# Kernel tuning notes

Hardware: AMD Instinct MI355X
Metric: run time of the kernel (lower is better)

The kernel has to match this reference:

```python
import jax, jax.numpy as jnp
import numpy as np
from jax import lax

EPS_CSA = 1e-5
EPS_BN = 1e-5


def _csa(x, w, pm_pos, ps_pos, pm_neg, ps_neg, label):
    # x: [B,C,H,W]; w: [B,K]; proto tables: [K,C]; label: [B] in {0,1}
    mean = jnp.mean(x, axis=(2, 3), keepdims=True)
    var = jnp.var(x, axis=(2, 3), ddof=1, keepdims=True)  # torch.var is unbiased
    mean = lax.stop_gradient(mean)
    var = lax.stop_gradient(var)
    x_norm = (x - mean) / jnp.sqrt(var + EPS_CSA)
    sel = (label == 0)[:, None]                       # [B,1]
    new_mean = jnp.where(sel, w @ pm_pos, w @ pm_neg)  # [B,C]
    new_std = jnp.where(sel, w @ ps_pos, w @ ps_neg)   # [B,C]
    return x_norm * new_std[:, :, None, None] + new_mean[:, :, None, None]


def _conv_bn(x, conv_w, gamma, beta):
    y = lax.conv_general_dilated(x, conv_w, (1, 1), 'SAME',
                                 dimension_numbers=('NCHW', 'OIHW', 'NCHW'))
    mu = jnp.mean(y, axis=(0, 2, 3), keepdims=True)
    var = jnp.var(y, axis=(0, 2, 3), keepdims=True)  # biased var, as BN training
    yn = (y - mu) / jnp.sqrt(var + EPS_BN)
    return yn * gamma[None, :, None, None] + beta[None, :, None, None]


def setup_inputs() -> dict:
    key = jax.random.key(0)
    ks = jax.random.split(key, 10)
    B, C, H, W, K, L = 32, 384, 32, 32, 64, 2
    conc = jnp.full((K,), 0.0156, dtype=jnp.float32)
    cw = jax.random.dirichlet(ks[5], conc, shape=(L, B)).astype(jnp.float32)
    return {
        'x': jax.random.normal(ks[0], (B, C, H, W), jnp.float32),
        'proto_mean_pos': jax.random.normal(ks[1], (L, K, C), jnp.float32),
        'proto_std_pos': jax.random.uniform(ks[2], (L, K, C), jnp.float32),
        'proto_mean_neg': jax.random.normal(ks[3], (L, K, C), jnp.float32),
        'proto_std_neg': jax.random.uniform(ks[4], (L, K, C), jnp.float32),
        'combine_weights': cw,
        'conv_w': jax.random.normal(ks[6], (C, C, 3, 3), jnp.float32) * (1.0 / np.sqrt(C * 9)),
        'bn_gamma': jnp.ones((C,), jnp.float32),
        'bn_beta': jnp.zeros((C,), jnp.float32),
        'label': jax.random.randint(ks[7], (B,), 0, 2, jnp.int32),
    }


def reference(x, proto_mean_pos, proto_std_pos, proto_mean_neg, proto_std_neg,
              combine_weights, conv_w, bn_gamma, bn_beta, label):
    fea = x
    for l in range(2):  # two CSABlocks: x + CSA(x, label)
        fea = fea + _csa(fea, combine_weights[l],
                         proto_mean_pos[l], proto_std_pos[l],
                         proto_mean_neg[l], proto_std_neg[l], label)
    out_feat = _conv_bn(fea, conv_w, bn_gamma, bn_beta)
    return out_feat
```

## Files before the change

kernel.cpp:

```cpp
#include <hip/hip_runtime.h>
#include <stdint.h>

using f32x4  = __attribute__((ext_vector_type(4))) float;
using short8 = __attribute__((ext_vector_type(8))) short;

#define DEVI static __device__ __forceinline__

DEVI unsigned short f2bf(float f) {
  unsigned u = __float_as_uint(f);
  u += 0x7FFFu + ((u >> 16) & 1u);
  return (unsigned short)(u >> 16);
}

DEVI void gld16(const void* g, void* l) {
  __builtin_amdgcn_global_load_lds(
      reinterpret_cast<const __attribute__((address_space(1))) unsigned int*>(
          reinterpret_cast<uintptr_t>(g)),
      reinterpret_cast<__attribute__((address_space(3))) unsigned int*>(
          reinterpret_cast<uintptr_t>(l)),
      16, 0, 0);
}

__global__ void k_zero(float* __restrict__ bn, float* __restrict__ zp) {
  const int t = threadIdx.x;
  for (int i = t; i < 768; i += 256) bn[i] = 0.0f;
  for (int i = t; i < 1024; i += 256) zp[i] = 0.0f;
}

__global__ __launch_bounds__(256) void k_stats(const float* __restrict__ x,
                                               float* __restrict__ sums,
                                               float* __restrict__ sumsq) {
  const int bc = blockIdx.x;
  const float4 v =
      reinterpret_cast<const float4*>(x + (size_t)bc * 1024)[threadIdx.x];
  float s = v.x + v.y + v.z + v.w;
  float q = v.x * v.x + v.y * v.y + v.z * v.z + v.w * v.w;
#pragma unroll
  for (int off = 1; off < 64; off <<= 1) {
    s += __shfl_xor(s, off, 64);
    q += __shfl_xor(q, off, 64);
  }
  __shared__ float ls[4], lq[4];
  const int wv = threadIdx.x >> 6;
  if ((threadIdx.x & 63) == 0) { ls[wv] = s; lq[wv] = q; }
  __syncthreads();
  if (threadIdx.x == 0) {
    sums[bc]  = ls[0] + ls[1] + ls[2] + ls[3];
    sumsq[bc] = lq[0] + lq[1] + lq[2] + lq[3];
  }
}

__global__ __launch_bounds__(384) void k_coef(
    const float* __restrict__ pmp, const float* __restrict__ psp,
    const float* __restrict__ pmn, const float* __restrict__ psn,
    const float* __restrict__ cw, const int* __restrict__ label,
    const float* __restrict__ sums, const float* __restrict__ sumsq,
    float* __restrict__ Ac, float* __restrict__ Bc) {
  const int b = blockIdx.x;
  const int c = threadIdx.x;
  __shared__ float w0[64], w1[64];
  if (threadIdx.x < 64) w0[threadIdx.x] = cw[b * 64 + threadIdx.x];
  else if (threadIdx.x < 128) w1[threadIdx.x - 64] = cw[2048 + b * 64 + (threadIdx.x - 64)];
  __syncthreads();
  const bool sel = (label[b] == 0);
  const float* m1t = (sel ? pmp : pmn);
  const float* s1t = (sel ? psp : psn);
  const float* m2t = m1t + 64 * 384;
  const float* s2t = s1t + 64 * 384;
  float m1 = 0.f, s1 = 0.f, m2 = 0.f, s2 = 0.f;
  for (int k = 0; k < 64; ++k) {
    const float a0 = w0[k], a1 = w1[k];
    m1 += a0 * m1t[k * 384 + c];
    s1 += a0 * s1t[k * 384 + c];
    m2 += a1 * m2t[k * 384 + c];
    s2 += a1 * s2t[k * 384 + c];
  }
  const int bc = b * 384 + c;
  const float sum = sums[bc], sq = sumsq[bc];
  const float mean = sum * (1.0f / 1024.0f);
  float var = (sq - sum * mean) * (1.0f / 1023.0f);
  var = fmaxf(var, 0.0f);
  const float sd1 = sqrtf(var + 1e-5f);
  const float a1c = 1.0f + s1 / sd1;
  const float b1c = m1 - mean * (s1 / sd1);
  const float mean1 = a1c * mean + b1c;
  const float var1  = a1c * a1c * var;
  const float sd2 = sqrtf(var1 + 1e-5f);
  const float t2 = 1.0f + s2 / sd2;
  Ac[bc] = a1c * t2;
  Bc[bc] = b1c * t2 + m2 - mean1 * (s2 / sd2);
}

__global__ __launch_bounds__(256) void k_fea(const float* __restrict__ x,
                                             const float* __restrict__ Ac,
                                             const float* __restrict__ Bc,
                                             unsigned short* __restrict__ fea) {
  __shared__ unsigned short tb[256][68];
  const int t = threadIdx.x;
  const int g0 = blockIdx.x << 8;
  const int b = g0 >> 10;
  const int c0 = blockIdx.y * 64;
  const float* xb = x + (((size_t)b * 384) << 10) + (g0 & 1023) + t;
  const float* Ab = Ac + b * 384 + c0;
  const float* Bb = Bc + b * 384 + c0;
#pragma unroll 1
  for (int u8 = 0; u8 < 64; u8 += 8) {
    union { unsigned short us[8]; uint4 v; } pk;
#pragma unroll
    for (int u = 0; u < 8; ++u) {
      const int c = u8 + u;
      pk.us[u] = f2bf(Ab[c] * xb[(size_t)(c0 + c) << 10] + Bb[c]);
    }
    *reinterpret_cast<uint4*>(&tb[t][u8]) = pk.v;
  }
  __syncthreads();
  const int j = t & 7;
#pragma unroll
  for (int rep = 0; rep < 8; ++rep) {
    const int p = rep * 32 + (t >> 3);
    const uint4 v = *reinterpret_cast<const uint4*>(&tb[p][j * 8]);
    *reinterpret_cast<uint4*>(fea + (size_t)(g0 + p) * 384 + c0 + j * 8) = v;
  }
}

__global__ __launch_bounds__(256) void k_wcvt(const float* __restrict__ w,
                                              unsigned short* __restrict__ wb2) {
  const int g = blockIdx.x * 256 + threadIdx.x;
  const int ct = g / 41472;
  const int r1 = g - ct * 41472;
  const int step = r1 / 1152;
  const int r2 = r1 - step * 1152;
  const int slab = r2 >> 6;
  const int lane = r2 & 63;
  const int cc = step / 3, dy = step - cc * 3;
  const int r = slab * 16 + (lane >> 2);
  const int dxl = r / 96, co_l = r - dxl * 96;
  const int dd = (lane & 3) ^ ((co_l >> 1) & 3);
  const int tap = dy * 3 + dxl;
  const int co = ct * 96 + co_l;
  const int cib = cc * 32 + dd * 8;
  union { unsigned short us[8]; uint4 v4; } pk;
#pragma unroll
  for (int u = 0; u < 8; ++u)
    pk.us[u] = f2bf(w[(size_t)(co * 384 + cib + u) * 9 + tap]);
  *reinterpret_cast<uint4*>(wb2 + (size_t)g * 8) = pk.v4;
}

__global__ __launch_bounds__(256, 1) void k_conv(
    const unsigned short* __restrict__ fea, const unsigned short* __restrict__ wb2,
    const unsigned short* __restrict__ zpg, float* __restrict__ out,
    float* __restrict__ bn_sum, float* __restrict__ bn_sq) {
  __shared__ __align__(16) unsigned char lds[129024];
  const int tid = threadIdx.x;
  const int lane = tid & 63, wv = tid >> 6;
  const int pt = blockIdx.x;
  const int ct = blockIdx.y;
  const int b = pt >> 1, h0 = (pt & 1) * 16;
  const int co0 = ct * 96;
  const int wn = wv;

  const int l15 = lane & 15, d = lane >> 4;
  const int aoff = l15 * 64 + ((d ^ ((l15 >> 1) & 3)) << 4);
  int baddr[8][3];
  bool ok0[8], ok2[8];
#pragma unroll
  for (int n = 0; n < 8; ++n) {
    const int p_out = wn * 128 + n * 16 + l15;
    const int r_out = p_out >> 5, c_out = p_out & 31;
    ok0[n] = (c_out >= 1);
    ok2[n] = (c_out <= 30);
#pragma unroll
    for (int dx = 0; dx < 3; ++dx) {
      const int c = c_out + dx - 1;
      const int cs = ((unsigned)c < 32u) ? c : c_out;
      const int row = r_out * 32 + cs;
      baddr[n][dx] = row * 64 + ((d ^ ((row >> 1) & 3)) << 4);
    }
  }

  const unsigned short* wp = wb2 + (size_t)ct * 331776 + lane * 8;
#define WSTAGE(wo)                                                  \
  do {                                                              \
    gld16(wp + wv * 512,          lds + (wo) + wv * 1024);          \
    gld16(wp + wv * 512 + 2048,   lds + (wo) + wv * 1024 + 4096);   \
    gld16(wp + wv * 512 + 4096,   lds + (wo) + wv * 1024 + 8192);   \
    gld16(wp + wv * 512 + 6144,   lds + (wo) + wv * 1024 + 12288);  \
    if (wv < 2)                                                     \
      gld16(wp + wv * 512 + 8192, lds + (wo) + wv * 1024 + 16384);  \
    wp += 9216;                                                     \
  } while (0)

  const unsigned short* ip[9];
  int istep[9];
#pragma unroll
  for (int dy2 = 0; dy2 < 3; ++dy2) {
#pragma unroll
    for (int k = 0; k < 3; ++k) {
      const int j = dy2 * 3 + k;
      const int s = dy2 * 12 + wv + 4 * k;
      const int pix = s * 16 + (lane >> 2);
      const int prow = pix >> 5, pcol = pix & 31;
      const int h = h0 - 1 + prow;
      const int dd = (lane & 3) ^ ((pix >> 1) & 3);
      if (h >= 0 && h < 32) {
        ip[j] = fea + ((size_t)((b * 32 + h) * 32 + pcol) * 384 + dd * 8);
        istep[j] = 32;
      } else {
        ip[j] = zpg + lane * 8;
        istep[j] = 0;
      }
    }
  }

  f32x4 acc[6][8] = {};
  const short8 z8 = {0, 0, 0, 0, 0, 0, 0, 0};
  short8 pf_af[6], pf_bf[8];

  WSTAGE(0);
  WSTAGE(18432);
#pragma unroll
  for (int j = 0; j < 9; ++j) {
    const int dy2 = j / 3, k = j - dy2 * 3;
    const int s = dy2 * 12 + wv + 4 * k;
    gld16(ip[j], lds + 55296 + s * 1024);
    ip[j] += istep[j];
  }
  __syncthreads();
#pragma unroll
  for (int m = 0; m < 6; ++m)
    pf_af[m] = *reinterpret_cast<const short8*>(lds + m * 1024 + aoff);

  for (int cc = 0; cc < 12; ++cc) {
#pragma unroll
    for (int dy = 0; dy < 3; ++dy) {
      const int st = cc * 3 + dy;
      const unsigned char* wbase = lds + dy * 18432;
      const unsigned char* wnext = lds + ((dy + 1) % 3) * 18432;
      const unsigned char* ibase = lds + 55296 + (cc & 1) * 36864;
      if (cc < 11 || dy == 0) WSTAGE(((dy + 2) % 3) * 18432);
      if (cc < 11) {
        const int io = 55296 + ((cc + 1) & 1) * 36864;
        const int s0 = dy * 12 + wv;
#pragma unroll
        for (int k = 0; k < 3; ++k) {
          const int j = dy * 3 + k;
          gld16(ip[j], lds + io + (s0 + 4 * k) * 1024);
          ip[j] += istep[j];
        }
      }
#pragma unroll
      for (int dx = 0; dx < 3; ++dx) {
        short8 af[6], bf[8];
        if (dx == 0) {
#pragma unroll
          for (int m = 0; m < 6; ++m) af[m] = pf_af[m];
          if (dy == 0) {
#pragma unroll
            for (int n = 0; n < 8; ++n) {
              short8 v = *reinterpret_cast<const short8*>(ibase + baddr[n][0]);
              bf[n] = ok0[n] ? v : z8;
            }
          } else {
#pragma unroll
            for (int n = 0; n < 8; ++n) bf[n] = pf_bf[n];
          }
        } else {
#pragma unroll
          for (int m = 0; m < 6; ++m)
            af[m] = *reinterpret_cast<const short8*>(
                wbase + dx * 6144 + m * 1024 + aoff);
#pragma unroll
          for (int n = 0; n < 8; ++n) {
            short8 v = *reinterpret_cast<const short8*>(
                ibase + baddr[n][dx] + dy * 2048);
            if (dx == 2) v = ok2[n] ? v : z8;
            bf[n] = v;
          }
        }
#pragma unroll
        for (int m = 0; m < 6; ++m)
#pragma unroll
          for (int n = 0; n < 8; ++n)
            acc[m][n] = __builtin_amdgcn_mfma_f32_16x16x32_bf16(
                af[m], bf[n], acc[m][n], 0, 0, 0);
      }
      if (st < 35) {
#pragma unroll
        for (int m = 0; m < 6; ++m)
          pf_af[m] = *reinterpret_cast<const short8*>(wnext + m * 1024 + aoff);
        if (dy < 2) {
#pragma unroll
          for (int n = 0; n < 8; ++n) {
            short8 v = *reinterpret_cast<const short8*>(
                ibase + baddr[n][0] + (dy + 1) * 2048);
            pf_bf[n] = ok0[n] ? v : z8;
          }
        }
      }
      __syncthreads();
    }
  }
#undef WSTAGE

  const size_t ob = (((size_t)b * 384 + co0) << 10) + h0 * 32;
#pragma unroll
  for (int m = 0; m < 6; ++m) {
#pragma unroll
    for (int r = 0; r < 4; ++r) {
      const int co = m * 16 + d * 4 + r;
      float s = 0.f, q = 0.f;
#pragma unroll
      for (int n = 0; n < 8; ++n) {
        const float v = acc[m][n][r];
        const int p = wn * 128 + n * 16 + l15;
        out[ob + ((size_t)co << 10) + p] = v;
        s += v; q += v * v;
      }
#pragma unroll
      for (int off = 1; off < 16; off <<= 1) {
        s += __shfl_xor(s, off, 64);
        q += __shfl_xor(q, off, 64);
      }
      if (l15 == 0) {
        atomicAdd(&bn_sum[co0 + co], s);
        atomicAdd(&bn_sq[co0 + co], q);
      }
    }
  }
}

__global__ __launch_bounds__(256) void k_bnfin(float* __restrict__ y,
                                               const float* __restrict__ bn_sum,
                                               const float* __restrict__ bn_sq,
                                               const float* __restrict__ gamma,
                                               const float* __restrict__ beta) {
  const size_t N4 = (size_t)32 * 384 * 1024 / 4;
  const float inv = 1.0f / 32768.0f;
  for (size_t i = (size_t)blockIdx.x * 256 + threadIdx.x; i < N4;
       i += (size_t)gridDim.x * 256) {
    const size_t e = i * 4;
    const int c = (int)((e >> 10) % 384);
    const float mu = bn_sum[c] * inv;
    const float var = fmaxf(bn_sq[c] * inv - mu * mu, 0.0f);
    const float rs = rsqrtf(var + 1e-5f) * gamma[c];
    const float bt = beta[c];
    float4 v = *reinterpret_cast<float4*>(y + e);
    v.x = (v.x - mu) * rs + bt;
    v.y = (v.y - mu) * rs + bt;
    v.z = (v.z - mu) * rs + bt;
    v.w = (v.w - mu) * rs + bt;
    *reinterpret_cast<float4*>(y + e) = v;
  }
}

extern "C" void kernel_launch(void* const* d_in, const int* in_sizes, int n_in,
                              void* d_out, int out_size, void* d_ws, size_t ws_size,
                              hipStream_t stream) {
  const float* x     = (const float*)d_in[0];
  const float* pmp   = (const float*)d_in[1];
  const float* psp   = (const float*)d_in[2];
  const float* pmn   = (const float*)d_in[3];
  const float* psn   = (const float*)d_in[4];
  const float* cw    = (const float*)d_in[5];
  const float* convw = (const float*)d_in[6];
  const float* gamma = (const float*)d_in[7];
  const float* beta  = (const float*)d_in[8];
  const int*   label = (const int*)d_in[9];
  float* out = (float*)d_out;
  char* ws = (char*)d_ws;

  unsigned short* fea = (unsigned short*)(ws);
  unsigned short* wb2 = (unsigned short*)(ws + 25165824);
  float* sums  = (float*)(ws + 27820032);
  float* sumsq = (float*)(ws + 27869184);
  float* Ac    = (float*)(ws + 27918336);
  float* Bc    = (float*)(ws + 27967488);
  float* bn    = (float*)(ws + 28016640);
  float* zp    = (float*)(ws + 28019712);

  k_zero<<<dim3(1), dim3(256), 0, stream>>>(bn, zp);
  k_stats<<<dim3(12288), dim3(256), 0, stream>>>(x, sums, sumsq);
  k_coef<<<dim3(32), dim3(384), 0, stream>>>(pmp, psp, pmn, psn, cw, label,
                                             sums, sumsq, Ac, Bc);
  k_fea<<<dim3(128, 6), dim3(256), 0, stream>>>(x, Ac, Bc, fea);
  k_wcvt<<<dim3(648), dim3(256), 0, stream>>>(convw, wb2);
  k_conv<<<dim3(64, 4), dim3(256), 0, stream>>>(fea, wb2, (const unsigned short*)zp,
                                                out, bn, bn + 384);
  k_bnfin<<<dim3(2048), dim3(256), 0, stream>>>(out, bn, bn + 384, gamma, beta);
}
```

Before: 161.6 us.

## Fuse BN finalize into conv via grid-wide counter barrier; fold zeroing into stats

The separate batch-norm finalize kernel is removed. Each conv block keeps its accumulators in registers, joins a per-channel-tile atomic counter barrier that waits for all 64 spatial blocks, then reads the completed channel sums and writes the normalized output directly. This drops one full write+read+write pass over the 50MB output and one launch. The zeroing kernel is also folded into the first block of the stats kernel. The spin barrier relies on all 256 blocks being co-resident (one block per CU with 256 CUs), so it risks deadlock or stalls if they are not.

```diff
diff --git a/kernel.cpp b/kernel.cpp
--- a/kernel.cpp
+++ b/kernel.cpp
@@ -21,16 +21,19 @@
       16, 0, 0);
 }
 
-__global__ void k_zero(float* __restrict__ bn, float* __restrict__ zp) {
-  const int t = threadIdx.x;
-  for (int i = t; i < 768; i += 256) bn[i] = 0.0f;
-  for (int i = t; i < 1024; i += 256) zp[i] = 0.0f;
-}
-
 __global__ __launch_bounds__(256) void k_stats(const float* __restrict__ x,
                                                float* __restrict__ sums,
-                                               float* __restrict__ sumsq) {
+                                               float* __restrict__ sumsq,
+                                               float* __restrict__ bn,
+                                               int* __restrict__ ctr,
+                                               float* __restrict__ zp) {
   const int bc = blockIdx.x;
+  if (bc == 0) {
+    const int t = threadIdx.x;
+    for (int i = t; i < 768; i += 256) bn[i] = 0.0f;
+    for (int i = t; i < 1024; i += 256) zp[i] = 0.0f;
+    if (t < 4) ctr[t] = 0;
+  }
   const float4 v =
       reinterpret_cast<const float4*>(x + (size_t)bc * 1024)[threadIdx.x];
   float s = v.x + v.y + v.z + v.w;
@@ -149,7 +152,9 @@
 __global__ __launch_bounds__(256, 1) void k_conv(
     const unsigned short* __restrict__ fea, const unsigned short* __restrict__ wb2,
     const unsigned short* __restrict__ zpg, float* __restrict__ out,
-    float* __restrict__ bn_sum, float* __restrict__ bn_sq) {
+    float* __restrict__ bn_sum, float* __restrict__ bn_sq,
+    const float* __restrict__ gamma, const float* __restrict__ beta,
+    int* __restrict__ ctr) {
   __shared__ __align__(16) unsigned char lds[129024];
   const int tid = threadIdx.x;
   const int lane = tid & 63, wv = tid >> 6;
@@ -302,7 +307,6 @@
   }
 #undef WSTAGE
 
-  const size_t ob = (((size_t)b * 384 + co0) << 10) + h0 * 32;
 #pragma unroll
   for (int m = 0; m < 6; ++m) {
 #pragma unroll
@@ -312,8 +316,6 @@
 #pragma unroll
       for (int n = 0; n < 8; ++n) {
         const float v = acc[m][n][r];
-        const int p = wn * 128 + n * 16 + l15;
-        out[ob + ((size_t)co << 10) + p] = v;
         s += v; q += v * v;
       }
 #pragma unroll
@@ -327,29 +329,47 @@
       }
     }
   }
-}
-
-__global__ __launch_bounds__(256) void k_bnfin(float* __restrict__ y,
-                                               const float* __restrict__ bn_sum,
-                                               const float* __restrict__ bn_sq,
-                                               const float* __restrict__ gamma,
-                                               const float* __restrict__ beta) {
-  const size_t N4 = (size_t)32 * 384 * 1024 / 4;
-  const float inv = 1.0f / 32768.0f;
-  for (size_t i = (size_t)blockIdx.x * 256 + threadIdx.x; i < N4;
-       i += (size_t)gridDim.x * 256) {
-    const size_t e = i * 4;
-    const int c = (int)((e >> 10) % 384);
-    const float mu = bn_sum[c] * inv;
-    const float var = fmaxf(bn_sq[c] * inv - mu * mu, 0.0f);
-    const float rs = rsqrtf(var + 1e-5f) * gamma[c];
-    const float bt = beta[c];
-    float4 v = *reinterpret_cast<float4*>(y + e);
-    v.x = (v.x - mu) * rs + bt;
-    v.y = (v.y - mu) * rs + bt;
-    v.z = (v.z - mu) * rs + bt;
-    v.w = (v.w - mu) * rs + bt;
-    *reinterpret_cast<float4*>(y + e) = v;
+
+  __threadfence();
+  __syncthreads();
+  if (tid == 0) atomicAdd(&ctr[ct], 1);
+  if (tid == 0) {
+    while (__hip_atomic_load(&ctr[ct], __ATOMIC_ACQUIRE,
+                             __HIP_MEMORY_SCOPE_AGENT) < 64)
+      __builtin_amdgcn_s_sleep(8);
+  }
+  __syncthreads();
+
+  float* ls_rs = reinterpret_cast<float*>(lds);
+  float* ls_bb = reinterpret_cast<float*>(lds + 512);
+  if (tid < 96) {
+    const int co = co0 + tid;
+    const float sv = __hip_atomic_load(&bn_sum[co], __ATOMIC_RELAXED,
+                                       __HIP_MEMORY_SCOPE_AGENT);
+    const float qv = __hip_atomic_load(&bn_sq[co], __ATOMIC_RELAXED,
+                                       __HIP_MEMORY_SCOPE_AGENT);
+    const float inv = 1.0f / 32768.0f;
+    const float mu = sv * inv;
+    const float var = fmaxf(qv * inv - mu * mu, 0.0f);
+    const float rs = rsqrtf(var + 1e-5f) * gamma[co];
+    ls_rs[tid] = rs;
+    ls_bb[tid] = beta[co] - mu * rs;
+  }
+  __syncthreads();
+
+  const size_t ob = (((size_t)b * 384 + co0) << 10) + h0 * 32;
+#pragma unroll
+  for (int m = 0; m < 6; ++m) {
+#pragma unroll
+    for (int r = 0; r < 4; ++r) {
+      const int co = m * 16 + d * 4 + r;
+      const float rs = ls_rs[co], bb = ls_bb[co];
+#pragma unroll
+      for (int n = 0; n < 8; ++n) {
+        const int p = wn * 128 + n * 16 + l15;
+        out[ob + ((size_t)co << 10) + p] = acc[m][n][r] * rs + bb;
+      }
+    }
   }
 }
 
@@ -377,14 +397,13 @@
   float* Bc    = (float*)(ws + 27967488);
   float* bn    = (float*)(ws + 28016640);
   float* zp    = (float*)(ws + 28019712);
-
-  k_zero<<<dim3(1), dim3(256), 0, stream>>>(bn, zp);
-  k_stats<<<dim3(12288), dim3(256), 0, stream>>>(x, sums, sumsq);
+  int*   ctr   = (int*)(ws + 28023808);
+
+  k_stats<<<dim3(12288), dim3(256), 0, stream>>>(x, sums, sumsq, bn, ctr, zp);
   k_coef<<<dim3(32), dim3(384), 0, stream>>>(pmp, psp, pmn, psn, cw, label,
                                              sums, sumsq, Ac, Bc);
   k_fea<<<dim3(128, 6), dim3(256), 0, stream>>>(x, Ac, Bc, fea);
   k_wcvt<<<dim3(648), dim3(256), 0, stream>>>(convw, wb2);
   k_conv<<<dim3(64, 4), dim3(256), 0, stream>>>(fea, wb2, (const unsigned short*)zp,
-                                                out, bn, bn + 384);
-  k_bnfin<<<dim3(2048), dim3(256), 0, stream>>>(out, bn, bn + 384, gamma, beta);
-}
+                                                out, bn, bn + 384, gamma, beta, ctr);
+}
```

Result: faster. 156.4 us (-3.2%).
